# Kernel optimization log

Measured on AMD Instinct MI355X. Metric: run time of the kernel, lower is better.

Reference implementation:

```python
import jax, jax.numpy as jnp
import numpy as np
import math

EMBED_DIM = 64
NUM_HEADS = 4
HEAD_DIM = EMBED_DIM // NUM_HEADS
TGT = 64
SRC = 64
BSZ = 128


def setup_inputs() -> dict:
    key = jax.random.key(0)
    ks = jax.random.split(key, 8)
    x = jax.random.normal(ks[0], (TGT, BSZ, EMBED_DIM), dtype=jnp.float32)
    relation = jax.random.normal(ks[1], (TGT, SRC, BSZ, EMBED_DIM), dtype=jnp.float32)
    in_proj_weight = jax.random.normal(ks[2], (3 * EMBED_DIM, EMBED_DIM), dtype=jnp.float32) * 0.02
    in_proj_bias = jnp.zeros((3 * EMBED_DIM,), dtype=jnp.float32)
    rel_weight = jax.random.normal(ks[3], (2 * EMBED_DIM, EMBED_DIM), dtype=jnp.float32) * 0.02
    rel_bias = jnp.zeros((2 * EMBED_DIM,), dtype=jnp.float32)
    out_weight = jax.random.normal(ks[4], (EMBED_DIM, EMBED_DIM), dtype=jnp.float32) * 0.02
    out_bias = jnp.zeros((EMBED_DIM,), dtype=jnp.float32)
    return {
        'query': x, 'key': x, 'value': x, 'relation': relation,
        'in_proj_weight': in_proj_weight, 'in_proj_bias': in_proj_bias,
        'rel_weight': rel_weight, 'rel_bias': rel_bias,
        'out_weight': out_weight, 'out_bias': out_bias,
    }


def reference(query, key, value, relation, in_proj_weight, in_proj_bias,
              rel_weight, rel_bias, out_weight, out_bias):
    E, H, hd = EMBED_DIM, NUM_HEADS, HEAD_DIM
    t, b, _ = query.shape
    s = key.shape[0]
    scaling = hd ** (-0.5)
    # qkv projections (slices of the fused in_proj weight, as in _in_proj)
    q = query @ in_proj_weight[:E].T + in_proj_bias[:E]
    k = key @ in_proj_weight[E:2 * E].T + in_proj_bias[E:2 * E]
    v = value @ in_proj_weight[2 * E:].T + in_proj_bias[2 * E:]
    q = q.reshape(t, b * H, hd)
    k = k.reshape(s, b * H, hd)
    v = v.reshape(s, b * H, hd)
    # relation projection -> ra, rb, each [t, s, b*H, hd], then transpose(0,1)
    rel = relation @ rel_weight.T + rel_bias  # [t, s, b, 2E]
    ra = rel[..., :E].reshape(t, s, b * H, hd).swapaxes(0, 1)  # [s, t, bH, hd]
    rb = rel[..., E:].reshape(t, s, b * H, hd).swapaxes(0, 1)
    # q[i,j] = q[i] + ra_t[i,j]; requires t == s (broadcast as in torch)
    qp = (q[:, None] + ra) * scaling            # [t, s, bH, hd]
    kp = k[None, :] + rb                        # [t, s, bH, hd]
    attn_weights = jnp.einsum('ijbn,ijbn->ijb', qp, kp) * (1.0 / math.sqrt(hd))
    attn_weights = jax.nn.softmax(attn_weights, axis=1)
    attn = jnp.einsum('ijb,jbn->bin', attn_weights, v)  # [bH, t, hd]
    attn = attn.swapaxes(0, 1).reshape(t, b, E)
    out = attn @ out_weight.T + out_bias
    return out
```

## Files before the change

### kernel.cpp

```cpp
#include <hip/hip_runtime.h>
#include <hip/hip_bf16.h>

#define T_ 64
#define S_ 64
#define B_ 128
#define E_ 64
#define H_ 4

typedef float f32x4 __attribute__((ext_vector_type(4)));
typedef short bf16x8 __attribute__((ext_vector_type(8)));

static __device__ __forceinline__ short f2b(float f) {
    union { __hip_bfloat16 h; short s; } u;
    u.h = __float2bfloat16(f);
    return u.s;
}

__global__ __launch_bounds__(256) void k_qkv(
    const float* __restrict__ qin, const float* __restrict__ kin,
    const float* __restrict__ vin, const float* __restrict__ W,
    const float* __restrict__ bias, float* __restrict__ qkv)
{
    __shared__ float xs[3][32 * 68];
    __shared__ float WTs[64 * 68];
    const int tid = threadIdx.x;
    const int row0 = blockIdx.x * 32;

    #pragma unroll
    for (int l = 0; l < 6; ++l) {
        int f4 = l * 256 + tid;
        int src = f4 >> 9, rem = f4 & 511;
        int r = rem >> 4, e0 = (rem & 15) << 2;
        const float* xin = (src == 0) ? qin : (src == 1 ? kin : vin);
        float4 xv = reinterpret_cast<const float4*>(xin)[(size_t)(row0 + r) * 16 + (e0 >> 2)];
        float* dst = &xs[src][r * 68];
        dst[e0] = xv.x; dst[e0 + 1] = xv.y; dst[e0 + 2] = xv.z; dst[e0 + 3] = xv.w;
    }

    const int rq = tid >> 5, og = tid & 31;
    const int r0 = rq * 4, op0 = og * 2;

    for (int seg = 0; seg < 3; ++seg) {
        __syncthreads();
        #pragma unroll
        for (int l = 0; l < 4; ++l) {
            int f4 = l * 256 + tid;
            int o = f4 >> 4, e0 = (f4 & 15) << 2;
            float4 wv = reinterpret_cast<const float4*>(W)[(size_t)(seg * 64 + o) * 16 + (e0 >> 2)];
            WTs[(e0 + 0) * 68 + o] = wv.x; WTs[(e0 + 1) * 68 + o] = wv.y;
            WTs[(e0 + 2) * 68 + o] = wv.z; WTs[(e0 + 3) * 68 + o] = wv.w;
        }
        __syncthreads();

        float acc[4][2];
        #pragma unroll
        for (int rr = 0; rr < 4; ++rr) {
            acc[rr][0] = bias[seg * 64 + op0];
            acc[rr][1] = bias[seg * 64 + op0 + 1];
        }
        const float* xsrc = xs[seg];
        #pragma unroll 4
        for (int e = 0; e < 64; ++e) {
            float w0 = WTs[e * 68 + op0];
            float w1 = WTs[e * 68 + op0 + 1];
            #pragma unroll
            for (int rr = 0; rr < 4; ++rr) {
                float xv = xsrc[(r0 + rr) * 68 + e];
                acc[rr][0] += xv * w0;
                acc[rr][1] += xv * w1;
            }
        }
        #pragma unroll
        for (int rr = 0; rr < 4; ++rr) {
            float2 ov = make_float2(acc[rr][0], acc[rr][1]);
            reinterpret_cast<float2*>(
                &qkv[((size_t)seg * T_ * B_ + row0 + r0 + rr) * E_ + op0])[0] = ov;
        }
    }
}

__global__ __launch_bounds__(512, 1) void k_logits_mfma(
    const float* __restrict__ rel, const float* __restrict__ relW,
    const float* __restrict__ relBias, const float* __restrict__ qkv,
    float* __restrict__ logits)
{
    __shared__ char  Bs[16384];
    __shared__ float llds[8][64][9];

    const int tid = threadIdx.x;
    const int w   = tid >> 6;
    const int l   = tid & 63;
    const int c   = l & 15;
    const int rq  = l >> 4;
    const int i   = blockIdx.x >> 3;
    const int jb  = (blockIdx.x & 7) * 8;

    #pragma unroll
    for (int li = 0; li < 4; ++li) {
        int f4 = li * 512 + tid;
        int o = f4 >> 4, e4 = f4 & 15;
        float4 wv = reinterpret_cast<const float4*>(relW)[f4];
        ushort4 bv;
        bv.x = (ushort)f2b(wv.x); bv.y = (ushort)f2b(wv.y);
        bv.z = (ushort)f2b(wv.z); bv.w = (ushort)f2b(wv.w);
        int ot = o >> 4, cc = o & 15;
        int ks = e4 >> 3, rqb = (e4 & 7) >> 1, half = e4 & 1;
        int dest = (ot * 2 + ks) * 1024 + (rqb * 16 + cc) * 16 + half * 8;
        *reinterpret_cast<ushort4*>(Bs + dest) = bv;
    }

    float qpre[4][4], bbv[4];
    {
        const float* qrow = qkv + (size_t)i * (B_ * E_);
        #pragma unroll
        for (int h = 0; h < 4; ++h) {
            float ba = relBias[h * 16 + c];
            bbv[h] = relBias[64 + h * 16 + c];
            #pragma unroll
            for (int r = 0; r < 4; ++r) {
                int b = w * 16 + rq * 4 + r;
                qpre[h][r] = qrow[b * E_ + h * 16 + c] + ba;
            }
        }
    }
    __syncthreads();

    bf16x8 bfr[8][2];
    #pragma unroll
    for (int ot = 0; ot < 8; ++ot)
        #pragma unroll
        for (int ks = 0; ks < 2; ++ks)
            bfr[ot][ks] = *(const bf16x8*)(Bs + (ot * 2 + ks) * 1024 + l * 16);

    const int arow = ((w * 16 + c) * E_) + rq * 8;
    const int kbase = (w * 16 + rq * 4) * E_;

#define LOADA(jj, X0, X1, X2, X3)                                              \
    {                                                                          \
        const float* ab = rel + ((size_t)(jj) * S_ + i) * (size_t)(B_ * E_) + arow; \
        X0 = *(const float4*)(ab);                                             \
        X1 = *(const float4*)(ab + 4);                                         \
        X2 = *(const float4*)(ab + 32);                                        \
        X3 = *(const float4*)(ab + 36);                                        \
    }

#define BODY(t, X0, X1, X2, X3)                                                \
    {                                                                          \
        const int j = jb + (t);                                                \
        float kvv[4][4];                                                       \
        {                                                                      \
            const float* krow = qkv + ((size_t)(T_ * B_) + (size_t)j * B_) * E_ + kbase; \
            _Pragma("unroll")                                                  \
            for (int h = 0; h < 4; ++h)                                        \
                _Pragma("unroll")                                              \
                for (int r = 0; r < 4; ++r)                                    \
                    kvv[h][r] = krow[r * E_ + h * 16 + c];                     \
        }                                                                      \
        bf16x8 af0, af1;                                                       \
        {                                                                      \
            bf16x8 a;                                                          \
            a[0] = f2b(X0.x); a[1] = f2b(X0.y); a[2] = f2b(X0.z); a[3] = f2b(X0.w); \
            a[4] = f2b(X1.x); a[5] = f2b(X1.y); a[6] = f2b(X1.z); a[7] = f2b(X1.w); \
            af0 = a;                                                           \
            a[0] = f2b(X2.x); a[1] = f2b(X2.y); a[2] = f2b(X2.z); a[3] = f2b(X2.w); \
            a[4] = f2b(X3.x); a[5] = f2b(X3.y); a[6] = f2b(X3.z); a[7] = f2b(X3.w); \
            af1 = a;                                                           \
        }                                                                      \
        if ((t) + 2 < 8) { LOADA(jb + (t) + 2, X0, X1, X2, X3) }               \
        f32x4 acc[8];                                                          \
        _Pragma("unroll")                                                      \
        for (int ot = 0; ot < 8; ++ot) acc[ot] = (f32x4){0.f, 0.f, 0.f, 0.f};  \
        _Pragma("unroll")                                                      \
        for (int ot = 0; ot < 8; ++ot) {                                       \
            acc[ot] = __builtin_amdgcn_mfma_f32_16x16x32_bf16(af0, bfr[ot][0], acc[ot], 0, 0, 0); \
            acc[ot] = __builtin_amdgcn_mfma_f32_16x16x32_bf16(af1, bfr[ot][1], acc[ot], 0, 0, 0); \
        }                                                                      \
        float v[16];                                                           \
        _Pragma("unroll")                                                      \
        for (int h = 0; h < 4; ++h)                                            \
            _Pragma("unroll")                                                  \
            for (int r = 0; r < 4; ++r)                                        \
                v[h * 4 + r] = (qpre[h][r] + acc[h][r]) *                      \
                               (kvv[h][r] + bbv[h] + acc[4 + h][r]);           \
        _Pragma("unroll")                                                      \
        for (int k = 0; k < 8; ++k) {                                          \
            float x = (c & 1) ? v[2 * k + 1] : v[2 * k];                       \
            float y = (c & 1) ? v[2 * k] : v[2 * k + 1];                       \
            v[k] = x + __shfl_xor(y, 1);                                       \
        }                                                                      \
        _Pragma("unroll")                                                      \
        for (int k = 0; k < 4; ++k) {                                          \
            float x = (c & 2) ? v[2 * k + 1] : v[2 * k];                       \
            float y = (c & 2) ? v[2 * k] : v[2 * k + 1];                       \
            v[k] = x + __shfl_xor(y, 2);                                       \
        }                                                                      \
        _Pragma("unroll")                                                      \
        for (int k = 0; k < 2; ++k) {                                          \
            float x = (c & 4) ? v[2 * k + 1] : v[2 * k];                       \
            float y = (c & 4) ? v[2 * k] : v[2 * k + 1];                       \
            v[k] = x + __shfl_xor(y, 4);                                       \
        }                                                                      \
        {                                                                      \
            float x = (c & 8) ? v[1] : v[0];                                   \
            float y = (c & 8) ? v[0] : v[1];                                   \
            llds[w][l][(t)] = (x + __shfl_xor(y, 8)) * 0.0625f;                \
        }                                                                      \
    }

    float4 aA0, aA1, aA2, aA3, aB0, aB1, aB2, aB3;
    LOADA(jb + 0, aA0, aA1, aA2, aA3)
    LOADA(jb + 1, aB0, aB1, aB2, aB3)

    #pragma unroll 1
    for (int tt = 0; tt < 8; tt += 2) {
        BODY(tt,     aA0, aA1, aA2, aA3)
        BODY(tt + 1, aB0, aB1, aB2, aB3)
    }
#undef BODY
#undef LOADA

    {
        float f[8];
        #pragma unroll
        for (int t2 = 0; t2 < 8; ++t2) f[t2] = llds[w][l][t2];
        const int hh = c >> 2, rr = c & 3;
        const int b = w * 16 + rq * 4 + rr;
        float* dst = &logits[(((size_t)i * B_ + b) * H_ + hh) * S_ + jb];
        *reinterpret_cast<float4*>(dst) = make_float4(f[0], f[1], f[2], f[3]);
        *reinterpret_cast<float4*>(dst + 4) = make_float4(f[4], f[5], f[6], f[7]);
    }
}

__global__ __launch_bounds__(256) void k_attn(
    const float* __restrict__ logits, const float* __restrict__ qkv,
    const float* __restrict__ Wout, const float* __restrict__ bout,
    float* __restrict__ out)
{
    __shared__ float wsm[4][H_][S_];
    __shared__ float ap[4][68];
    const int tid = threadIdx.x;
    const int i = blockIdx.x >> 5;
    const int bq = blockIdx.x & 31;
    const int w = tid >> 6, l = tid & 63;
    const int b = bq * 4 + w;

    const float* lg = logits + ((size_t)i * B_ + b) * H_ * S_;
    const int h = l >> 4, sub = l & 15;
    float v0 = lg[h * S_ + sub];
    float v1 = lg[h * S_ + sub + 16];
    float v2 = lg[h * S_ + sub + 32];
    float v3 = lg[h * S_ + sub + 48];
    float m = fmaxf(fmaxf(v0, v1), fmaxf(v2, v3));
    #pragma unroll
    for (int d = 1; d < 16; d <<= 1) m = fmaxf(m, __shfl_xor(m, d));
    float e0 = expf(v0 - m), e1 = expf(v1 - m), e2 = expf(v2 - m), e3 = expf(v3 - m);
    float ss = e0 + e1 + e2 + e3;
    #pragma unroll
    for (int d = 1; d < 16; d <<= 1) ss += __shfl_xor(ss, d);
    float inv = 1.0f / ss;
    wsm[w][h][sub] = e0 * inv;
    wsm[w][h][sub + 16] = e1 * inv;
    wsm[w][h][sub + 32] = e2 * inv;
    wsm[w][h][sub + 48] = e3 * inv;
    __syncthreads();

    const float* vbase = qkv + (size_t)2 * T_ * B_ * E_ + (size_t)b * E_;
    const float* wrow = &wsm[w][l >> 4][0];
    float acc = 0.f;
    #pragma unroll 4
    for (int j = 0; j < S_; ++j) acc += wrow[j] * vbase[(size_t)j * B_ * E_ + l];
    ap[w][l] = acc;
    __syncthreads();

    const float* wo = Wout + l * E_;
    const float* apw = ap[w];
    float oacc = bout[l];
    #pragma unroll 4
    for (int e = 0; e < E_; ++e) oacc += apw[e] * wo[e];
    out[((size_t)i * B_ + b) * E_ + l] = oacc;
}

extern "C" void kernel_launch(void* const* d_in, const int* in_sizes, int n_in,
                              void* d_out, int out_size, void* d_ws, size_t ws_size,
                              hipStream_t stream)
{
    const float* qin = (const float*)d_in[0];
    const float* kin = (const float*)d_in[1];
    const float* vin = (const float*)d_in[2];
    const float* rel = (const float*)d_in[3];
    const float* ipw = (const float*)d_in[4];
    const float* ipb = (const float*)d_in[5];
    const float* rw  = (const float*)d_in[6];
    const float* rb  = (const float*)d_in[7];
    const float* ow  = (const float*)d_in[8];
    const float* obias = (const float*)d_in[9];

    float* qkv = (float*)d_ws;
    float* logits = qkv + 3 * T_ * B_ * E_;
    float* out = (float*)d_out;

    k_qkv<<<dim3(256), dim3(256), 0, stream>>>(qin, kin, vin, ipw, ipb, qkv);
    k_logits_mfma<<<dim3(512), dim3(512), 0, stream>>>(rel, rw, rb, qkv, logits);
    k_attn<<<dim3(2048), dim3(256), 0, stream>>>(logits, qkv, ow, obias, out);
}
```

Baseline: 70.24 us.

## Stage relation tiles via async LDS loads and fold key+bias into MFMA

The relation-weight bf16 conversion moves into an extra block of the QKV kernel, which writes a pre-swizzled bf16 weight image plus identity tiles. The same kernel writes a bf16 copy of k plus the relation bias in MFMA fragment layout. The logits kernel now runs 1024-thread blocks that double-buffer relation tiles into XOR-swizzled LDS with global_load_lds. It reads B fragments from LDS on each use instead of holding them in registers, and adds k plus bias through an extra MFMA against the identity tile. This removes per-block weight conversion and scalar k loads and overlaps HBM streaming with compute. In exchange it rounds k plus bias to bf16 and relies on hand-set vmcnt waits.

```diff
diff --git a/kernel.cpp b/kernel.cpp
--- a/kernel.cpp
+++ b/kernel.cpp
@@ -19,11 +19,39 @@
 __global__ __launch_bounds__(256) void k_qkv(
     const float* __restrict__ qin, const float* __restrict__ kin,
     const float* __restrict__ vin, const float* __restrict__ W,
-    const float* __restrict__ bias, float* __restrict__ qkv)
+    const float* __restrict__ bias, float* __restrict__ qkv,
+    const float* __restrict__ relW, const float* __restrict__ relBias,
+    ushort* __restrict__ wBf, unsigned int* __restrict__ kpbW)
 {
+    const int tid = threadIdx.x;
+
+    if (blockIdx.x == 256) {
+        #pragma unroll
+        for (int li = 0; li < 8; ++li) {
+            int f4 = li * 256 + tid;
+            int o = f4 >> 4, e4 = f4 & 15;
+            float4 wv = reinterpret_cast<const float4*>(relW)[f4];
+            ushort4 bv;
+            bv.x = (ushort)f2b(wv.x); bv.y = (ushort)f2b(wv.y);
+            bv.z = (ushort)f2b(wv.z); bv.w = (ushort)f2b(wv.w);
+            int ot = o >> 4, cc = o & 15;
+            int ks = e4 >> 3, rqb = (e4 & 7) >> 1, half = e4 & 1;
+            int dest = (ot * 2 + ks) * 512 + (rqb * 16 + cc) * 8 + half * 4;
+            *reinterpret_cast<ushort4*>(wBf + dest) = bv;
+        }
+        #pragma unroll
+        for (int li = 0; li < 8; ++li) {
+            int t = li * 256 + tid;
+            int ot = t >> 9, lane = (t >> 3) & 63, e = t & 7;
+            int cI = lane & 15, rqI = lane >> 4;
+            wBf[8192 + t] =
+                (rqI * 8 + e == (ot & 1) * 16 + cI) ? (ushort)0x3F80 : (ushort)0;
+        }
+        return;
+    }
+
     __shared__ float xs[3][32 * 68];
     __shared__ float WTs[64 * 68];
-    const int tid = threadIdx.x;
     const int row0 = blockIdx.x * 32;
 
     #pragma unroll
@@ -76,112 +104,127 @@
             reinterpret_cast<float2*>(
                 &qkv[((size_t)seg * T_ * B_ + row0 + r0 + rr) * E_ + op0])[0] = ov;
         }
-    }
-}
-
-__global__ __launch_bounds__(512, 1) void k_logits_mfma(
-    const float* __restrict__ rel, const float* __restrict__ relW,
-    const float* __restrict__ relBias, const float* __restrict__ qkv,
-    float* __restrict__ logits)
+        if (seg == 1) {
+            #pragma unroll
+            for (int rr = 0; rr < 4; ++rr) {
+                int row = row0 + r0 + rr;
+                int jj = row >> 7, b = row & 127;
+                float kb0 = acc[rr][0] + relBias[64 + op0];
+                float kb1 = acc[rr][1] + relBias[64 + op0 + 1];
+                unsigned int u = (unsigned int)(ushort)f2b(kb0) |
+                                 ((unsigned int)(ushort)f2b(kb1) << 16);
+                int off = jj * 8192 + (op0 >> 5) * 4096 + (b >> 4) * 512 +
+                          ((b & 15) + ((op0 & 31) >> 3) * 16) * 8 + (op0 & 7);
+                kpbW[off >> 1] = u;
+            }
+        }
+    }
+}
+
+__global__ __launch_bounds__(1024, 1) void k_logits_mfma(
+    const float* __restrict__ rel, const ushort* __restrict__ wBf,
+    const ushort* __restrict__ kpbF, const float* __restrict__ relBias,
+    const float* __restrict__ qkv, float* __restrict__ logits)
 {
-    __shared__ char  Bs[16384];
-    __shared__ float llds[8][64][9];
+    __shared__ char Bs[20480];
+    __shared__ char As[131072];
 
     const int tid = threadIdx.x;
-    const int w   = tid >> 6;
-    const int l   = tid & 63;
-    const int c   = l & 15;
-    const int rq  = l >> 4;
-    const int i   = blockIdx.x >> 3;
-    const int jb  = (blockIdx.x & 7) * 8;
-
-    #pragma unroll
-    for (int li = 0; li < 4; ++li) {
-        int f4 = li * 512 + tid;
-        int o = f4 >> 4, e4 = f4 & 15;
-        float4 wv = reinterpret_cast<const float4*>(relW)[f4];
-        ushort4 bv;
-        bv.x = (ushort)f2b(wv.x); bv.y = (ushort)f2b(wv.y);
-        bv.z = (ushort)f2b(wv.z); bv.w = (ushort)f2b(wv.w);
-        int ot = o >> 4, cc = o & 15;
-        int ks = e4 >> 3, rqb = (e4 & 7) >> 1, half = e4 & 1;
-        int dest = (ot * 2 + ks) * 1024 + (rqb * 16 + cc) * 16 + half * 8;
-        *reinterpret_cast<ushort4*>(Bs + dest) = bv;
-    }
-
-    float qpre[4][4], bbv[4];
+    const int W = tid >> 6, l = tid & 63;
+    const int w = W & 7;
+    const int c = l & 15, rq = l >> 4;
+    const int i  = blockIdx.x >> 2;
+    const int jb = (blockIdx.x & 3) * 16 + (W >> 3) * 8;
+
+    for (int idx = tid; idx < 1280; idx += 1024)
+        reinterpret_cast<float4*>(Bs)[idx] =
+            reinterpret_cast<const float4*>(wBf)[idx];
+
+    float qpre[4][4];
     {
         const float* qrow = qkv + (size_t)i * (B_ * E_);
         #pragma unroll
         for (int h = 0; h < 4; ++h) {
             float ba = relBias[h * 16 + c];
-            bbv[h] = relBias[64 + h * 16 + c];
             #pragma unroll
-            for (int r = 0; r < 4; ++r) {
-                int b = w * 16 + rq * 4 + r;
-                qpre[h][r] = qrow[b * E_ + h * 16 + c] + ba;
-            }
+            for (int r = 0; r < 4; ++r)
+                qpre[h][r] = qrow[(w * 16 + rq * 4 + r) * E_ + h * 16 + c] + ba;
         }
     }
     __syncthreads();
 
-    bf16x8 bfr[8][2];
-    #pragma unroll
-    for (int ot = 0; ot < 8; ++ot)
-        #pragma unroll
-        for (int ks = 0; ks < 2; ++ks)
-            bfr[ot][ks] = *(const bf16x8*)(Bs + (ot * 2 + ks) * 1024 + l * 16);
-
-    const int arow = ((w * 16 + c) * E_) + rq * 8;
-    const int kbase = (w * 16 + rq * 4) * E_;
-
-#define LOADA(jj, X0, X1, X2, X3)                                              \
+    char* Asw = As + W * 8192;
+    const int lr = l >> 4, lu = l & 15;
+    const int kfo = w * 512 + l * 8;
+
+#define STAGE(jj, bufi)                                                        \
     {                                                                          \
-        const float* ab = rel + ((size_t)(jj) * S_ + i) * (size_t)(B_ * E_) + arow; \
-        X0 = *(const float4*)(ab);                                             \
-        X1 = *(const float4*)(ab + 4);                                         \
-        X2 = *(const float4*)(ab + 32);                                        \
-        X3 = *(const float4*)(ab + 36);                                        \
-    }
-
-#define BODY(t, X0, X1, X2, X3)                                                \
+        const char* srcb = (const char*)(rel + ((size_t)(jj) * S_ + i) * (size_t)(B_ * E_)); \
+        char* dstb = Asw + (bufi) * 4096;                                      \
+        _Pragma("unroll")                                                      \
+        for (int it = 0; it < 4; ++it) {                                       \
+            int r = it * 4 + lr;                                               \
+            int srcoff = (w * 16 + r) * 256 + ((lu ^ (r & 7)) << 4);           \
+            __builtin_amdgcn_global_load_lds(                                  \
+                (const __attribute__((address_space(1))) void*)(srcb + srcoff),\
+                (__attribute__((address_space(3))) void*)(dstb + it * 1024),   \
+                16, 0, 0);                                                     \
+        }                                                                      \
+    }
+
+#define BODY(T, NSTR)                                                          \
     {                                                                          \
-        const int j = jb + (t);                                                \
-        float kvv[4][4];                                                       \
-        {                                                                      \
-            const float* krow = qkv + ((size_t)(T_ * B_) + (size_t)j * B_) * E_ + kbase; \
-            _Pragma("unroll")                                                  \
-            for (int h = 0; h < 4; ++h)                                        \
-                _Pragma("unroll")                                              \
-                for (int r = 0; r < 4; ++r)                                    \
-                    kvv[h][r] = krow[r * E_ + h * 16 + c];                     \
-        }                                                                      \
+        if ((T) < 7) {                                                         \
+            STAGE(jb + (T) + 1, ((T) & 1) ^ 1)                                 \
+            kfa_n = *(const bf16x8*)(kpbF + (size_t)(jb + (T) + 1) * 8192 + kfo);        \
+            kfb_n = *(const bf16x8*)(kpbF + (size_t)(jb + (T) + 1) * 8192 + 4096 + kfo); \
+        }                                                                      \
+        asm volatile("s_waitcnt vmcnt(" NSTR ")" ::: "memory");                \
+        const char* abase = Asw + ((T) & 1) * 4096 + c * 256;                  \
+        const int s7 = c & 7;                                                  \
+        float4 x0 = *(const float4*)(abase + (((rq * 2 + 0) ^ s7) << 4));      \
+        float4 x1 = *(const float4*)(abase + (((rq * 2 + 1) ^ s7) << 4));      \
+        float4 x2 = *(const float4*)(abase + (((8 + rq * 2 + 0) ^ s7) << 4));  \
+        float4 x3 = *(const float4*)(abase + (((8 + rq * 2 + 1) ^ s7) << 4));  \
         bf16x8 af0, af1;                                                       \
         {                                                                      \
             bf16x8 a;                                                          \
-            a[0] = f2b(X0.x); a[1] = f2b(X0.y); a[2] = f2b(X0.z); a[3] = f2b(X0.w); \
-            a[4] = f2b(X1.x); a[5] = f2b(X1.y); a[6] = f2b(X1.z); a[7] = f2b(X1.w); \
+            a[0] = f2b(x0.x); a[1] = f2b(x0.y); a[2] = f2b(x0.z); a[3] = f2b(x0.w); \
+            a[4] = f2b(x1.x); a[5] = f2b(x1.y); a[6] = f2b(x1.z); a[7] = f2b(x1.w); \
             af0 = a;                                                           \
-            a[0] = f2b(X2.x); a[1] = f2b(X2.y); a[2] = f2b(X2.z); a[3] = f2b(X2.w); \
-            a[4] = f2b(X3.x); a[5] = f2b(X3.y); a[6] = f2b(X3.z); a[7] = f2b(X3.w); \
+            a[0] = f2b(x2.x); a[1] = f2b(x2.y); a[2] = f2b(x2.z); a[3] = f2b(x2.w); \
+            a[4] = f2b(x3.x); a[5] = f2b(x3.y); a[6] = f2b(x3.z); a[7] = f2b(x3.w); \
             af1 = a;                                                           \
         }                                                                      \
-        if ((t) + 2 < 8) { LOADA(jb + (t) + 2, X0, X1, X2, X3) }               \
+        int bs0 = 0;                                                           \
+        asm volatile("" : "+v"(bs0));                                          \
+        const char* bsp = Bs + bs0;                                            \
         f32x4 acc[8];                                                          \
         _Pragma("unroll")                                                      \
-        for (int ot = 0; ot < 8; ++ot) acc[ot] = (f32x4){0.f, 0.f, 0.f, 0.f};  \
-        _Pragma("unroll")                                                      \
-        for (int ot = 0; ot < 8; ++ot) {                                       \
-            acc[ot] = __builtin_amdgcn_mfma_f32_16x16x32_bf16(af0, bfr[ot][0], acc[ot], 0, 0, 0); \
-            acc[ot] = __builtin_amdgcn_mfma_f32_16x16x32_bf16(af1, bfr[ot][1], acc[ot], 0, 0, 0); \
+        for (int ot = 0; ot < 8; ++ot) acc[ot] = (f32x4){0.f, 0.f, 0.f, 0.f}; \
+        _Pragma("unroll")                                                      \
+        for (int ot = 0; ot < 4; ++ot) {                                       \
+            acc[ot] = __builtin_amdgcn_mfma_f32_16x16x32_bf16(                 \
+                af0, *(const bf16x8*)(bsp + (ot * 2 + 0) * 1024 + l * 16), acc[ot], 0, 0, 0); \
+            acc[ot] = __builtin_amdgcn_mfma_f32_16x16x32_bf16(                 \
+                af1, *(const bf16x8*)(bsp + (ot * 2 + 1) * 1024 + l * 16), acc[ot], 0, 0, 0); \
+        }                                                                      \
+        _Pragma("unroll")                                                      \
+        for (int ot = 0; ot < 4; ++ot) {                                       \
+            acc[4 + ot] = __builtin_amdgcn_mfma_f32_16x16x32_bf16(             \
+                af0, *(const bf16x8*)(bsp + (8 + ot * 2 + 0) * 1024 + l * 16), acc[4 + ot], 0, 0, 0); \
+            acc[4 + ot] = __builtin_amdgcn_mfma_f32_16x16x32_bf16(             \
+                af1, *(const bf16x8*)(bsp + (8 + ot * 2 + 1) * 1024 + l * 16), acc[4 + ot], 0, 0, 0); \
+            acc[4 + ot] = __builtin_amdgcn_mfma_f32_16x16x32_bf16(             \
+                (ot < 2 ? kfa : kfb),                                          \
+                *(const bf16x8*)(bsp + (16 + ot) * 1024 + l * 16), acc[4 + ot], 0, 0, 0); \
         }                                                                      \
         float v[16];                                                           \
         _Pragma("unroll")                                                      \
         for (int h = 0; h < 4; ++h)                                            \
             _Pragma("unroll")                                                  \
             for (int r = 0; r < 4; ++r)                                        \
-                v[h * 4 + r] = (qpre[h][r] + acc[h][r]) *                      \
-                               (kvv[h][r] + bbv[h] + acc[4 + h][r]);           \
+                v[h * 4 + r] = (qpre[h][r] + acc[h][r]) * acc[4 + h][r];       \
         _Pragma("unroll")                                                      \
         for (int k = 0; k < 8; ++k) {                                          \
             float x = (c & 1) ? v[2 * k + 1] : v[2 * k];                       \
@@ -203,31 +246,28 @@
         {                                                                      \
             float x = (c & 8) ? v[1] : v[0];                                   \
             float y = (c & 8) ? v[0] : v[1];                                   \
-            llds[w][l][(t)] = (x + __shfl_xor(y, 8)) * 0.0625f;                \
-        }                                                                      \
-    }
-
-    float4 aA0, aA1, aA2, aA3, aB0, aB1, aB2, aB3;
-    LOADA(jb + 0, aA0, aA1, aA2, aA3)
-    LOADA(jb + 1, aB0, aB1, aB2, aB3)
-
-    #pragma unroll 1
-    for (int tt = 0; tt < 8; tt += 2) {
-        BODY(tt,     aA0, aA1, aA2, aA3)
-        BODY(tt + 1, aB0, aB1, aB2, aB3)
-    }
+            lbuf[(T)] = (x + __shfl_xor(y, 8)) * 0.0625f;                      \
+        }                                                                      \
+        if ((T) < 7) { kfa = kfa_n; kfb = kfb_n; }                             \
+    }
+
+    STAGE(jb, 0)
+    bf16x8 kfa = *(const bf16x8*)(kpbF + (size_t)jb * 8192 + kfo);
+    bf16x8 kfb = *(const bf16x8*)(kpbF + (size_t)jb * 8192 + 4096 + kfo);
+    bf16x8 kfa_n = kfa, kfb_n = kfb;
+    float lbuf[8];
+
+    BODY(0, "6") BODY(1, "6") BODY(2, "6") BODY(3, "6")
+    BODY(4, "6") BODY(5, "6") BODY(6, "6") BODY(7, "0")
 #undef BODY
-#undef LOADA
+#undef STAGE
 
     {
-        float f[8];
-        #pragma unroll
-        for (int t2 = 0; t2 < 8; ++t2) f[t2] = llds[w][l][t2];
         const int hh = c >> 2, rr = c & 3;
         const int b = w * 16 + rq * 4 + rr;
         float* dst = &logits[(((size_t)i * B_ + b) * H_ + hh) * S_ + jb];
-        *reinterpret_cast<float4*>(dst) = make_float4(f[0], f[1], f[2], f[3]);
-        *reinterpret_cast<float4*>(dst + 4) = make_float4(f[4], f[5], f[6], f[7]);
+        *reinterpret_cast<float4*>(dst) = make_float4(lbuf[0], lbuf[1], lbuf[2], lbuf[3]);
+        *reinterpret_cast<float4*>(dst + 4) = make_float4(lbuf[4], lbuf[5], lbuf[6], lbuf[7]);
     }
 }
 
@@ -297,9 +337,13 @@
 
     float* qkv = (float*)d_ws;
     float* logits = qkv + 3 * T_ * B_ * E_;
+    ushort* wBf  = (ushort*)(logits + (size_t)T_ * S_ * B_ * H_);
+    ushort* kpbF = wBf + 16384;
+
     float* out = (float*)d_out;
 
-    k_qkv<<<dim3(256), dim3(256), 0, stream>>>(qin, kin, vin, ipw, ipb, qkv);
-    k_logits_mfma<<<dim3(512), dim3(512), 0, stream>>>(rel, rw, rb, qkv, logits);
+    k_qkv<<<dim3(257), dim3(256), 0, stream>>>(qin, kin, vin, ipw, ipb, qkv,
+                                               rw, rb, wBf, (unsigned int*)kpbF);
+    k_logits_mfma<<<dim3(256), dim3(1024), 0, stream>>>(rel, wBf, kpbF, rb, qkv, logits);
     k_attn<<<dim3(2048), dim3(256), 0, stream>>>(logits, qkv, ow, obias, out);
 }
```

Result: slower. 165.4 us (+135.5%).
